# Kernel optimization log

Measured on AMD Instinct MI355X. Metric: run time of the kernel, lower is better.

The kernel has to match this reference:

```python
import jax, jax.numpy as jnp
import numpy as np


def setup_inputs() -> dict:
    key = jax.random.key(0)
    k1, k2 = jax.random.split(key)
    B, D, T_ENC, T_DEC = 16, 256, 512, 2048
    x = jax.random.normal(k1, (B, D, T_ENC), dtype=jnp.float32)
    path = jax.random.uniform(k2, (B, T_ENC, T_DEC), dtype=jnp.float32)
    return {"x": x, "path": path}


def reference(x, path):
    # Batched matmul: [B, D, T_enc] @ [B, T_enc, T_dec] -> [B, D, T_dec]
    return jnp.einsum('bde,bet->bdt', x, path)
```

## Files before the change

### kernel.cpp

```cpp
#include <hip/hip_runtime.h>
#include <hip/hip_bf16.h>

#define NB 16
#define ND 256
#define NK 512
#define NT 2048

#define BM 128
#define BN 64
#define BK 32
#define RSA 40
#define RSB 36
#define KITERS (NK / BK)

typedef __attribute__((ext_vector_type(8))) short short8;
typedef __attribute__((ext_vector_type(4))) float f32x4;

union S8U { short8 v; uint2 u[2]; };
union BF2U { __hip_bfloat162 h; unsigned int u; };

__device__ inline unsigned int pack2bf(float a, float b) {
    BF2U c; c.h = __float22bfloat162_rn(make_float2(a, b));
    return c.u;
}

__global__ __launch_bounds__(256, 4)
void bmm_bf16_mfma(const float* __restrict__ x, const float* __restrict__ path,
                   float* __restrict__ out) {
    const int n0 = blockIdx.x * BN;
    const int m0 = blockIdx.y * BM;
    const int b  = blockIdx.z;
    const int t    = threadIdx.x;
    const int lane = t & 63;
    const int wv   = t >> 6;
    const int wr   = (wv >> 1) * 64;
    const int wc   = (wv & 1) * 32;
    const int q    = lane >> 4;
    const int lm   = lane & 15;

    __shared__ unsigned short As[2][BM * RSA];
    __shared__ unsigned short Bs[2][BN * RSB];

    const float* xg = x    + ((size_t)b * ND + m0) * NK;
    const float* pg = path + (size_t)b * NK * NT + n0;

    f32x4 acc[4][2];
#pragma unroll
    for (int i = 0; i < 4; ++i)
#pragma unroll
        for (int j = 0; j < 2; ++j)
            acc[i][j] = (f32x4){0.f, 0.f, 0.f, 0.f};

    float4 aReg[4];
    float  bReg[8];

#define LOAD_TILE(k0)                                                         \
    {                                                                         \
        _Pragma("unroll")                                                     \
        for (int i = 0; i < 4; ++i) {                                         \
            int f = t + i * 256;                                              \
            int row = f >> 3, c4 = f & 7;                                     \
            aReg[i] = *reinterpret_cast<const float4*>(                       \
                xg + (size_t)row * NK + (k0) + c4 * 4);                       \
        }                                                                     \
        _Pragma("unroll")                                                     \
        for (int j = 0; j < 8; ++j)                                           \
            bReg[j] = pg[(size_t)((k0) + wv * 8 + j) * NT + lane];            \
    }

#define STORE_TILE(buf)                                                       \
    {                                                                         \
        _Pragma("unroll")                                                     \
        for (int i = 0; i < 4; ++i) {                                         \
            int f = t + i * 256;                                              \
            int row = f >> 3, c4 = f & 7;                                     \
            uint2 p;                                                          \
            p.x = pack2bf(aReg[i].x, aReg[i].y);                              \
            p.y = pack2bf(aReg[i].z, aReg[i].w);                              \
            *reinterpret_cast<uint2*>(&As[buf][row * RSA + c4 * 4]) = p;      \
        }                                                                     \
        uint2 pk0, pk1;                                                       \
        pk0.x = pack2bf(bReg[0], bReg[1]);                                    \
        pk0.y = pack2bf(bReg[2], bReg[3]);                                    \
        pk1.x = pack2bf(bReg[4], bReg[5]);                                    \
        pk1.y = pack2bf(bReg[6], bReg[7]);                                    \
        *reinterpret_cast<uint2*>(&Bs[buf][lane * RSB + wv * 8]) = pk0;       \
        *reinterpret_cast<uint2*>(&Bs[buf][lane * RSB + wv * 8 + 4]) = pk1;   \
    }

    LOAD_TILE(0)
    STORE_TILE(0)
    __syncthreads();

    for (int it = 0; it < KITERS; ++it) {
        const int cur = it & 1;
        if (it + 1 < KITERS) LOAD_TILE((it + 1) * BK)

        short8 af[4];
        short8 bfr[2];
#pragma unroll
        for (int mt = 0; mt < 4; ++mt) {
            int row = wr + mt * 16 + lm;
            af[mt] = *reinterpret_cast<const short8*>(&As[cur][row * RSA + q * 8]);
        }
#pragma unroll
        for (int nt = 0; nt < 2; ++nt) {
            int n = wc + nt * 16 + lm;
            S8U s;
            s.u[0] = *reinterpret_cast<const uint2*>(&Bs[cur][n * RSB + q * 8]);
            s.u[1] = *reinterpret_cast<const uint2*>(&Bs[cur][n * RSB + q * 8 + 4]);
            bfr[nt] = s.v;
        }
#pragma unroll
        for (int mt = 0; mt < 4; ++mt)
#pragma unroll
            for (int nt = 0; nt < 2; ++nt)
                acc[mt][nt] = __builtin_amdgcn_mfma_f32_16x16x32_bf16(
                    af[mt], bfr[nt], acc[mt][nt], 0, 0, 0);

        if (it + 1 < KITERS) STORE_TILE(1 - cur)
        __syncthreads();
    }

    float* og = out + ((size_t)b * ND + m0 + wr) * NT + n0 + wc;
#pragma unroll
    for (int mt = 0; mt < 4; ++mt) {
#pragma unroll
        for (int r = 0; r < 4; ++r) {
            int row = mt * 16 + q * 4 + r;
#pragma unroll
            for (int nt = 0; nt < 2; ++nt) {
                int col = nt * 16 + lm;
                og[(size_t)row * NT + col] = acc[mt][nt][r];
            }
        }
    }
}

extern "C" void kernel_launch(void* const* d_in, const int* in_sizes, int n_in,
                              void* d_out, int out_size, void* d_ws, size_t ws_size,
                              hipStream_t stream) {
    const float* x    = (const float*)d_in[0];
    const float* path = (const float*)d_in[1];
    float* out        = (float*)d_out;
    dim3 grid(NT / BN, ND / BM, NB);
    dim3 block(256);
    bmm_bf16_mfma<<<grid, block, 0, stream>>>(x, path, out);
}
```

Baseline: 130.8 us.

## Enlarge block tile to 128x128x64 with 64x64 per-wave MFMA tiles

Doubles the N tile to 128 and the K tile to 64, so each wave computes a 64x64 output subtile with 16 MFMA accumulators. The main loop is restructured with a peeled final iteration and kept rolled. The goal is more operand reuse per LDS read and per global load, and fewer barriers and K iterations. The cost is higher register and LDS use, occupancy lowered to 2 blocks per SM, and half as many blocks (512), which may fill the GPU less well.

```diff
diff --git a/kernel.cpp b/kernel.cpp
--- a/kernel.cpp
+++ b/kernel.cpp
@@ -5,13 +5,12 @@
 #define ND 256
 #define NK 512
 #define NT 2048
-
 #define BM 128
-#define BN 64
-#define BK 32
-#define RSA 40
-#define RSB 36
+#define BN 128
+#define BK 64
 #define KITERS (NK / BK)
+#define RSA 72
+#define RSB 68
 
 typedef __attribute__((ext_vector_type(8))) short short8;
 typedef __attribute__((ext_vector_type(4))) float f32x4;
@@ -24,7 +23,7 @@
     return c.u;
 }
 
-__global__ __launch_bounds__(256, 4)
+__global__ __launch_bounds__(256, 2)
 void bmm_bf16_mfma(const float* __restrict__ x, const float* __restrict__ path,
                    float* __restrict__ out) {
     const int n0 = blockIdx.x * BN;
@@ -33,8 +32,8 @@
     const int t    = threadIdx.x;
     const int lane = t & 63;
     const int wv   = t >> 6;
-    const int wr   = (wv >> 1) * 64;
-    const int wc   = (wv & 1) * 32;
+    const int wm   = (wv >> 1) * 64;
+    const int wn   = (wv & 1) * 64;
     const int q    = lane >> 4;
     const int lm   = lane & 15;
 
@@ -44,97 +43,106 @@
     const float* xg = x    + ((size_t)b * ND + m0) * NK;
     const float* pg = path + (size_t)b * NK * NT + n0;
 
-    f32x4 acc[4][2];
+    f32x4 acc[4][4];
 #pragma unroll
     for (int i = 0; i < 4; ++i)
 #pragma unroll
-        for (int j = 0; j < 2; ++j)
+        for (int j = 0; j < 4; ++j)
             acc[i][j] = (f32x4){0.f, 0.f, 0.f, 0.f};
 
-    float4 aReg[4];
-    float  bReg[8];
+    float4 aR[8];
+    float  bR[32];
 
 #define LOAD_TILE(k0)                                                         \
     {                                                                         \
         _Pragma("unroll")                                                     \
-        for (int i = 0; i < 4; ++i) {                                         \
+        for (int i = 0; i < 8; ++i) {                                         \
             int f = t + i * 256;                                              \
-            int row = f >> 3, c4 = f & 7;                                     \
-            aReg[i] = *reinterpret_cast<const float4*>(                       \
+            int row = f >> 4, c4 = f & 15;                                    \
+            aR[i] = *reinterpret_cast<const float4*>(                         \
                 xg + (size_t)row * NK + (k0) + c4 * 4);                       \
         }                                                                     \
         _Pragma("unroll")                                                     \
-        for (int j = 0; j < 8; ++j)                                           \
-            bReg[j] = pg[(size_t)((k0) + wv * 8 + j) * NT + lane];            \
+        for (int j = 0; j < 16; ++j) {                                        \
+            const float* s = pg + (size_t)((k0) + wv * 16 + j) * NT + lane;   \
+            bR[j]      = s[0];                                                \
+            bR[16 + j] = s[64];                                               \
+        }                                                                     \
     }
 
 #define STORE_TILE(buf)                                                       \
     {                                                                         \
         _Pragma("unroll")                                                     \
-        for (int i = 0; i < 4; ++i) {                                         \
+        for (int i = 0; i < 8; ++i) {                                         \
             int f = t + i * 256;                                              \
-            int row = f >> 3, c4 = f & 7;                                     \
+            int row = f >> 4, c4 = f & 15;                                    \
             uint2 p;                                                          \
-            p.x = pack2bf(aReg[i].x, aReg[i].y);                              \
-            p.y = pack2bf(aReg[i].z, aReg[i].w);                              \
+            p.x = pack2bf(aR[i].x, aR[i].y);                                  \
+            p.y = pack2bf(aR[i].z, aR[i].w);                                  \
             *reinterpret_cast<uint2*>(&As[buf][row * RSA + c4 * 4]) = p;      \
         }                                                                     \
-        uint2 pk0, pk1;                                                       \
-        pk0.x = pack2bf(bReg[0], bReg[1]);                                    \
-        pk0.y = pack2bf(bReg[2], bReg[3]);                                    \
-        pk1.x = pack2bf(bReg[4], bReg[5]);                                    \
-        pk1.y = pack2bf(bReg[6], bReg[7]);                                    \
-        *reinterpret_cast<uint2*>(&Bs[buf][lane * RSB + wv * 8]) = pk0;       \
-        *reinterpret_cast<uint2*>(&Bs[buf][lane * RSB + wv * 8 + 4]) = pk1;   \
+        _Pragma("unroll")                                                     \
+        for (int g = 0; g < 4; ++g) {                                         \
+            uint2 p0, p1;                                                     \
+            p0.x = pack2bf(bR[4 * g + 0], bR[4 * g + 1]);                     \
+            p0.y = pack2bf(bR[4 * g + 2], bR[4 * g + 3]);                     \
+            p1.x = pack2bf(bR[16 + 4 * g + 0], bR[16 + 4 * g + 1]);           \
+            p1.y = pack2bf(bR[16 + 4 * g + 2], bR[16 + 4 * g + 3]);           \
+            *reinterpret_cast<uint2*>(&Bs[buf][lane * RSB + wv * 16 + 4 * g]) = p0; \
+            *reinterpret_cast<uint2*>(&Bs[buf][(lane + 64) * RSB + wv * 16 + 4 * g]) = p1; \
+        }                                                                     \
+    }
+
+#define MFMA_TILE(buf)                                                        \
+    {                                                                         \
+        _Pragma("unroll")                                                     \
+        for (int kc = 0; kc < 2; ++kc) {                                      \
+            short8 af[4], bfr[4];                                             \
+            _Pragma("unroll")                                                 \
+            for (int mt = 0; mt < 4; ++mt)                                    \
+                af[mt] = *reinterpret_cast<const short8*>(                    \
+                    &As[buf][(wm + mt * 16 + lm) * RSA + kc * 32 + q * 8]);   \
+            _Pragma("unroll")                                                 \
+            for (int nt = 0; nt < 4; ++nt) {                                  \
+                S8U s;                                                        \
+                const unsigned short* bp =                                    \
+                    &Bs[buf][(wn + nt * 16 + lm) * RSB + kc * 32 + q * 8];    \
+                s.u[0] = *reinterpret_cast<const uint2*>(bp);                 \
+                s.u[1] = *reinterpret_cast<const uint2*>(bp + 4);             \
+                bfr[nt] = s.v;                                                \
+            }                                                                 \
+            _Pragma("unroll")                                                 \
+            for (int mt = 0; mt < 4; ++mt)                                    \
+                _Pragma("unroll")                                             \
+                for (int nt = 0; nt < 4; ++nt)                                \
+                    acc[mt][nt] = __builtin_amdgcn_mfma_f32_16x16x32_bf16(    \
+                        af[mt], bfr[nt], acc[mt][nt], 0, 0, 0);               \
+        }                                                                     \
     }
 
     LOAD_TILE(0)
     STORE_TILE(0)
     __syncthreads();
 
-    for (int it = 0; it < KITERS; ++it) {
-        const int cur = it & 1;
-        if (it + 1 < KITERS) LOAD_TILE((it + 1) * BK)
-
-        short8 af[4];
-        short8 bfr[2];
-#pragma unroll
-        for (int mt = 0; mt < 4; ++mt) {
-            int row = wr + mt * 16 + lm;
-            af[mt] = *reinterpret_cast<const short8*>(&As[cur][row * RSA + q * 8]);
-        }
-#pragma unroll
-        for (int nt = 0; nt < 2; ++nt) {
-            int n = wc + nt * 16 + lm;
-            S8U s;
-            s.u[0] = *reinterpret_cast<const uint2*>(&Bs[cur][n * RSB + q * 8]);
-            s.u[1] = *reinterpret_cast<const uint2*>(&Bs[cur][n * RSB + q * 8 + 4]);
-            bfr[nt] = s.v;
-        }
-#pragma unroll
-        for (int mt = 0; mt < 4; ++mt)
-#pragma unroll
-            for (int nt = 0; nt < 2; ++nt)
-                acc[mt][nt] = __builtin_amdgcn_mfma_f32_16x16x32_bf16(
-                    af[mt], bfr[nt], acc[mt][nt], 0, 0, 0);
-
-        if (it + 1 < KITERS) STORE_TILE(1 - cur)
+#pragma unroll 1
+    for (int it = 0; it < KITERS - 1; ++it) {
+        LOAD_TILE((it + 1) * BK)
+        MFMA_TILE(it & 1)
+        STORE_TILE((it + 1) & 1)
         __syncthreads();
     }
+    MFMA_TILE((KITERS - 1) & 1)
 
-    float* og = out + ((size_t)b * ND + m0 + wr) * NT + n0 + wc;
+    float* og = out + ((size_t)b * ND + (m0 + wm)) * NT + n0 + wn;
 #pragma unroll
-    for (int mt = 0; mt < 4; ++mt) {
+    for (int mt = 0; mt < 4; ++mt)
 #pragma unroll
         for (int r = 0; r < 4; ++r) {
             int row = mt * 16 + q * 4 + r;
 #pragma unroll
-            for (int nt = 0; nt < 2; ++nt) {
-                int col = nt * 16 + lm;
-                og[(size_t)row * NT + col] = acc[mt][nt][r];
-            }
+            for (int nt = 0; nt < 4; ++nt)
+                og[(size_t)row * NT + nt * 16 + lm] = acc[mt][nt][r];
         }
-    }
 }
 
 extern "C" void kernel_launch(void* const* d_in, const int* in_sizes, int n_in,
```

Measured after the change: 122.1 us. 1.07x faster.
